# Kernel optimization log

Measured on AMD Instinct MI355X. Metric: run time of the kernel, lower is better.

## Reference

```python
import jax, jax.numpy as jnp
import numpy as np

N = 4096   # query tokens
M = 4096   # key/value tokens
D = 512    # embedding_dim


def setup_inputs() -> dict:
    key = jax.random.key(0)
    kq, kk, kv = jax.random.split(key, 3)
    return {
        "query": jax.random.normal(kq, (N, D), dtype=jnp.float32),
        "key": jax.random.normal(kk, (M, D), dtype=jnp.float32),
        "value": jax.random.normal(kv, (M, D), dtype=jnp.float32),
    }


def reference(query, key, value):
    # scores = Q K^T  (no 1/sqrt(d) scaling in the original module)
    attention_scores = jnp.einsum("nd,md->nm", query, key)  # [N, M]
    attention_probs = jax.nn.softmax(attention_scores, axis=-1)  # [N, M]
    output = jnp.einsum("nm,md->nd", attention_probs, value)  # [N, D]
    return (output, attention_probs)
```

## Files before the change

kernel.cpp:

```cpp
#include <hip/hip_runtime.h>
#include <hip/hip_bf16.h>
#include <stdint.h>

#define N_Q 4096
#define N_K 4096
#define DIM 512

typedef float f32x4 __attribute__((ext_vector_type(4)));
typedef __bf16 bf16x8 __attribute__((ext_vector_type(8)));
typedef unsigned short u16x4 __attribute__((ext_vector_type(4)));
typedef unsigned short u16x8 __attribute__((ext_vector_type(8)));

__device__ __forceinline__ f32x4 mfma_bf16(bf16x8 a, bf16x8 b, f32x4 c) {
  return __builtin_amdgcn_mfma_f32_16x16x32_bf16(a, b, c, 0, 0, 0);
}

__device__ __forceinline__ void gload16(const void* g, void* l) {
  __builtin_amdgcn_global_load_lds((const __attribute__((address_space(1))) void*)g,
                                   (__attribute__((address_space(3))) void*)l,
                                   16, 0, 0);
}

__device__ __forceinline__ void split4(const f32x4 v, u16x4& h, u16x4& l) {
#pragma unroll
  for (int i = 0; i < 4; ++i) {
    float f = v[i];
    uint32_t u = __builtin_bit_cast(uint32_t, f);
    uint32_t hb = (u + 0x8000u) & 0xffff0000u;
    float hf = __builtin_bit_cast(float, hb);
    float lf = f - hf;
    h[i] = (unsigned short)(hb >> 16);
    l[i] = (unsigned short)(__builtin_bit_cast(uint32_t, lf) >> 16);
  }
}

__device__ __forceinline__ unsigned short bf16r(float f) {
  uint32_t u = __builtin_bit_cast(uint32_t, f);
  return (unsigned short)((u + 0x8000u) >> 16);
}

__global__ __launch_bounds__(256) void split_kernel(const float* __restrict__ X,
                                                    unsigned short* __restrict__ X2) {
  const size_t base = ((size_t)blockIdx.x * 256 + threadIdx.x) * 8;
  const size_t row = base >> 9;
  const size_t col = base & 511;
  u16x8 H, L;
#pragma unroll
  for (int h = 0; h < 2; ++h) {
    f32x4 v = *(const f32x4*)(X + base + h * 4);
    u16x4 hh, ll;
    split4(v, hh, ll);
#pragma unroll
    for (int j = 0; j < 4; ++j) { H[h * 4 + j] = hh[j]; L[h * 4 + j] = ll[j]; }
  }
  *(u16x8*)(X2 + row * 1024 + col) = H;
  *(u16x8*)(X2 + row * 1024 + 512 + col) = L;
}

__global__ __launch_bounds__(256, 2) void qk2_kernel(const unsigned short* __restrict__ Xq,
                                                     const unsigned short* __restrict__ Xk,
                                                     float* __restrict__ S) {
  __shared__ __align__(16) char smem[65536];

  const int tid = threadIdx.x;
  const int lane = tid & 63, wid = tid >> 6;
  const int wr = wid >> 1, wc = wid & 1;

  const int bid = blockIdx.x;
  const int b = (bid & 7) * 128 + (bid >> 3);
  const int rbase = (b >> 5) * 128;
  const int cbase = (b & 31) * 128;

  const int lrow = lane >> 3;
  const int lchk = lane & 7;

  const f32x4 fzero = {0.f, 0.f, 0.f, 0.f};
  f32x4 acc[4][4];
#pragma unroll
  for (int m = 0; m < 4; ++m)
#pragma unroll
    for (int n = 0; n < 4; ++n) acc[m][n] = fzero;

  auto stage = [&](int buf, int t) {
#pragma unroll
    for (int i = 0; i < 4; ++i) {
      const int r = (wid << 5) + (i << 3) + lrow;
      const int sc = lchk ^ (r & 7);
      const unsigned short* g =
          Xq + (size_t)(rbase + r) * 1024 + (sc >> 2) * 512 + t * 32 + (sc & 3) * 8;
      uint32_t off = (uint32_t)(buf * 32768 + (((wid << 5) + (i << 3)) << 7));
      off = (uint32_t)__builtin_amdgcn_readfirstlane((int)off);
      gload16(g, smem + off);
    }
#pragma unroll
    for (int i = 0; i < 4; ++i) {
      const int r = (wid << 5) + (i << 3) + lrow;
      const int sc = lchk ^ (r & 7);
      const unsigned short* g =
          Xk + (size_t)(cbase + r) * 1024 + (sc >> 2) * 512 + t * 32 + (sc & 3) * 8;
      uint32_t off = (uint32_t)(buf * 32768 + 16384 + (((wid << 5) + (i << 3)) << 7));
      off = (uint32_t)__builtin_amdgcn_readfirstlane((int)off);
      gload16(g, smem + off);
    }
  };

  auto compute = [&](int buf) {
    const char* bA = smem + buf * 32768;
    const char* bB = bA + 16384;
    bf16x8 ah[4], al[4], bh[4], bl[4];
#pragma unroll
    for (int m = 0; m < 4; ++m) {
      int row = (wr << 6) + (m << 4) + (lane & 15);
      int ch = (lane >> 4) ^ (row & 7);
      int cl = (4 + (lane >> 4)) ^ (row & 7);
      ah[m] = *(const bf16x8*)(bA + row * 128 + ch * 16);
      al[m] = *(const bf16x8*)(bA + row * 128 + cl * 16);
    }
#pragma unroll
    for (int n = 0; n < 4; ++n) {
      int row = (wc << 6) + (n << 4) + (lane & 15);
      int ch = (lane >> 4) ^ (row & 7);
      int cl = (4 + (lane >> 4)) ^ (row & 7);
      bh[n] = *(const bf16x8*)(bB + row * 128 + ch * 16);
      bl[n] = *(const bf16x8*)(bB + row * 128 + cl * 16);
    }
#pragma unroll
    for (int m = 0; m < 4; ++m)
#pragma unroll
      for (int n = 0; n < 4; ++n) {
        acc[m][n] = mfma_bf16(ah[m], bh[n], acc[m][n]);
        acc[m][n] = mfma_bf16(ah[m], bl[n], acc[m][n]);
        acc[m][n] = mfma_bf16(al[m], bh[n], acc[m][n]);
      }
  };

  stage(0, 0);
  __syncthreads();
  int cur = 0;
  for (int t = 0; t < 16; ++t) {
    if (t + 1 < 16) stage(cur ^ 1, t + 1);
    compute(cur);
    __syncthreads();
    cur ^= 1;
  }

#pragma unroll
  for (int m = 0; m < 4; ++m) {
    int row = rbase + wr * 64 + m * 16 + (lane >> 4) * 4;
#pragma unroll
    for (int n = 0; n < 4; ++n) {
      int col = cbase + wc * 64 + n * 16 + (lane & 15);
#pragma unroll
      for (int j = 0; j < 4; ++j)
        S[(size_t)(row + j) * N_K + col] = acc[m][n][j];
    }
  }
}

__global__ __launch_bounds__(256, 2) void qk_kernel(const float* __restrict__ Q,
                                                    const float* __restrict__ K,
                                                    float* __restrict__ S) {
  __shared__ __align__(16) char sAh[16384];
  __shared__ __align__(16) char sAl[16384];
  __shared__ __align__(16) char sBh[16384];
  __shared__ __align__(16) char sBl[16384];

  const int tid = threadIdx.x;
  const int rbase = blockIdx.y * 128;
  const int cbase = blockIdx.x * 128;
  const int lane = tid & 63, wid = tid >> 6;
  const int wr = wid >> 1, wc = wid & 1;
  const int lr = lane & 15, lk = (lane >> 4) * 8;

  const int srow = tid >> 4;
  const int scol = (tid & 15) * 4;

  f32x4 qr[8], kr[8];
#pragma unroll
  for (int p = 0; p < 8; ++p) {
    int r = p * 16 + srow;
    qr[p] = *(const f32x4*)(Q + (size_t)(rbase + r) * DIM + scol);
    kr[p] = *(const f32x4*)(K + (size_t)(cbase + r) * DIM + scol);
  }

  const f32x4 fzero = {0.f, 0.f, 0.f, 0.f};
  f32x4 acc[4][4];
#pragma unroll
  for (int m = 0; m < 4; ++m)
#pragma unroll
    for (int n = 0; n < 4; ++n) acc[m][n] = fzero;

  for (int kk = 0; kk < DIM / 64; ++kk) {
    __syncthreads();
#pragma unroll
    for (int p = 0; p < 8; ++p) {
      int r = p * 16 + srow;
      uint32_t bo = (uint32_t)(r * 128) + (uint32_t)((scol * 2) ^ ((r & 7) << 4));
      u16x4 qh, ql, kh, kl;
      split4(qr[p], qh, ql);
      split4(kr[p], kh, kl);
      *(u16x4*)(sAh + bo) = qh;
      *(u16x4*)(sAl + bo) = ql;
      *(u16x4*)(sBh + bo) = kh;
      *(u16x4*)(sBl + bo) = kl;
    }
    __syncthreads();
    if (kk < DIM / 64 - 1) {
#pragma unroll
      for (int p = 0; p < 8; ++p) {
        int r = p * 16 + srow;
        qr[p] = *(const f32x4*)(Q + (size_t)(rbase + r) * DIM + (kk + 1) * 64 + scol);
        kr[p] = *(const f32x4*)(K + (size_t)(cbase + r) * DIM + (kk + 1) * 64 + scol);
      }
    }
#pragma unroll
    for (int kh = 0; kh < 2; ++kh) {
      bf16x8 a_h[4], a_l[4], b_h[4], b_l[4];
#pragma unroll
      for (int m = 0; m < 4; ++m) {
        int row = wr * 64 + m * 16 + lr;
        uint32_t co = (uint32_t)(((kh * 32 + lk) * 2) ^ ((row & 7) << 4));
        a_h[m] = *(const bf16x8*)(sAh + row * 128 + co);
        a_l[m] = *(const bf16x8*)(sAl + row * 128 + co);
      }
#pragma unroll
      for (int n = 0; n < 4; ++n) {
        int row = wc * 64 + n * 16 + lr;
        uint32_t co = (uint32_t)(((kh * 32 + lk) * 2) ^ ((row & 7) << 4));
        b_h[n] = *(const bf16x8*)(sBh + row * 128 + co);
        b_l[n] = *(const bf16x8*)(sBl + row * 128 + co);
      }
#pragma unroll
      for (int m = 0; m < 4; ++m)
#pragma unroll
        for (int n = 0; n < 4; ++n) {
          acc[m][n] = mfma_bf16(a_h[m], b_h[n], acc[m][n]);
          acc[m][n] = mfma_bf16(a_h[m], b_l[n], acc[m][n]);
          acc[m][n] = mfma_bf16(a_l[m], b_h[n], acc[m][n]);
        }
    }
  }

#pragma unroll
  for (int m = 0; m < 4; ++m) {
    int row = rbase + wr * 64 + m * 16 + (lane >> 4) * 4;
#pragma unroll
    for (int n = 0; n < 4; ++n) {
      int col = cbase + wc * 64 + n * 16 + lr;
#pragma unroll
      for (int j = 0; j < 4; ++j)
        S[(size_t)(row + j) * N_K + col] = acc[m][n][j];
    }
  }
}

__global__ __launch_bounds__(256) void softmax_kernel(float* __restrict__ P,
                                                      unsigned short* __restrict__ Pb) {
  const int tid = threadIdx.x;
  const int wid = tid >> 6, lane = tid & 63;
  float* p = P + (size_t)blockIdx.x * N_K;

  f32x4 v[4];
  float mx = -3.0e38f;
#pragma unroll
  for (int i = 0; i < 4; ++i) {
    v[i] = *(const f32x4*)(p + i * 1024 + tid * 4);
    mx = fmaxf(mx, fmaxf(fmaxf(v[i][0], v[i][1]), fmaxf(v[i][2], v[i][3])));
  }
#pragma unroll
  for (int o = 32; o > 0; o >>= 1) mx = fmaxf(mx, __shfl_xor(mx, o, 64));
  __shared__ float redM[4];
  __shared__ float redS[4];
  if (lane == 0) redM[wid] = mx;
  __syncthreads();
  mx = fmaxf(fmaxf(redM[0], redM[1]), fmaxf(redM[2], redM[3]));

  float s = 0.f;
#pragma unroll
  for (int i = 0; i < 4; ++i) {
#pragma unroll
    for (int j = 0; j < 4; ++j) {
      v[i][j] = __expf(v[i][j] - mx);
      s += v[i][j];
    }
  }
#pragma unroll
  for (int o = 32; o > 0; o >>= 1) s += __shfl_xor(s, o, 64);
  if (lane == 0) redS[wid] = s;
  __syncthreads();
  s = redS[0] + redS[1] + redS[2] + redS[3];
  const float inv = 1.0f / s;

  unsigned short* pb = Pb ? (Pb + (size_t)blockIdx.x * N_K) : nullptr;
#pragma unroll
  for (int i = 0; i < 4; ++i) {
    v[i] *= inv;
    *(f32x4*)(p + i * 1024 + tid * 4) = v[i];
    if (pb) {
      u16x4 h;
#pragma unroll
      for (int j = 0; j < 4; ++j) h[j] = bf16r(v[i][j]);
      *(u16x4*)(pb + i * 1024 + tid * 4) = h;
    }
  }
}

__global__ __launch_bounds__(256) void vt_kernel(const float* __restrict__ V,
                                                 unsigned short* __restrict__ Vt) {
  __shared__ unsigned short t[64][72];
  const int tid = threadIdx.x;
  const int d0 = blockIdx.x * 64;
  const int k0 = blockIdx.y * 64;

#pragma unroll
  for (int c = 0; c < 4; ++c) {
    int kr = (tid >> 4) + c * 16;
    f32x4 v = *(const f32x4*)(V + (size_t)(k0 + kr) * DIM + d0 + (tid & 15) * 4);
#pragma unroll
    for (int j = 0; j < 4; ++j) t[(tid & 15) * 4 + j][kr] = bf16r(v[j]);
  }
  __syncthreads();
#pragma unroll
  for (int c = 0; c < 2; ++c) {
    int d = (tid >> 3) + c * 32;
    int k = (tid & 7) * 8;
    *(uint4*)(Vt + (size_t)(d0 + d) * N_K + k0 + k) = *(const uint4*)&t[d][k];
  }
}

__global__ __launch_bounds__(256, 2) void pv3_kernel(const unsigned short* __restrict__ Pb,
                                                     const unsigned short* __restrict__ Vt,
                                                     float* __restrict__ Opart,
                                                     int kspan) {
  __shared__ __align__(16) char smem[65536];

  const int tid = threadIdx.x;
  const int lane = tid & 63, wid = tid >> 6;
  const int wr = wid >> 1, wc = wid & 1;
  const int rbase = blockIdx.y * 128;
  const int cbase = blockIdx.x * 128;
  const int k0 = blockIdx.z * kspan;
  float* Out = Opart + (size_t)blockIdx.z * ((size_t)N_Q * DIM);

  const int lrow = lane >> 3;
  const int lchk = lane & 7;
  const int iters = kspan >> 6;

  const f32x4 fzero = {0.f, 0.f, 0.f, 0.f};
  f32x4 acc[4][4];
#pragma unroll
  for (int m = 0; m < 4; ++m)
#pragma unroll
    for (int n = 0; n < 4; ++n) acc[m][n] = fzero;

  auto stage = [&](int buf, int t) {
    const size_t kel = (size_t)k0 + ((size_t)t << 6);
#pragma unroll
    for (int i = 0; i < 4; ++i) {
      const int rr = (wid << 5) + (i << 3) + lrow;
      const int gc = lchk ^ (rr & 7);
      const void* gA = (const void*)(Pb + (size_t)(rbase + rr) * N_K + kel + (gc << 3));
      uint32_t off = (uint32_t)(buf * 32768 + (((wid << 5) + (i << 3)) << 7));
      off = (uint32_t)__builtin_amdgcn_readfirstlane((int)off);
      gload16(gA, smem + off);
    }
#pragma unroll
    for (int i = 0; i < 4; ++i) {
      const int rr = (wid << 5) + (i << 3) + lrow;
      const int gc = lchk ^ (rr & 7);
      const void* gB = (const void*)(Vt + (size_t)(cbase + rr) * N_K + kel + (gc << 3));
      uint32_t off = (uint32_t)(buf * 32768 + 16384 + (((wid << 5) + (i << 3)) << 7));
      off = (uint32_t)__builtin_amdgcn_readfirstlane((int)off);
      gload16(gB, smem + off);
    }
  };

  auto compute = [&](int buf) {
    const char* bA = smem + buf * 32768;
    const char* bB = bA + 16384;
#pragma unroll
    for (int kh = 0; kh < 2; ++kh) {
      bf16x8 a[4], b[4];
#pragma unroll
      for (int m = 0; m < 4; ++m) {
        int row = (wr << 6) + (m << 4) + (lane & 15);
        uint32_t co = (uint32_t)(((((kh << 2) + (lane >> 4)) << 4)) ^ ((row & 7) << 4));
        a[m] = *(const bf16x8*)(bA + row * 128 + co);
      }
#pragma unroll
      for (int n = 0; n < 4; ++n) {
        int row = (wc << 6) + (n << 4) + (lane & 15);
        uint32_t co = (uint32_t)(((((kh << 2) + (lane >> 4)) << 4)) ^ ((row & 7) << 4));
        b[n] = *(const bf16x8*)(bB + row * 128 + co);
      }
#pragma unroll
      for (int m = 0; m < 4; ++m)
#pragma unroll
        for (int n = 0; n < 4; ++n)
          acc[m][n] = mfma_bf16(a[m], b[n], acc[m][n]);
    }
  };

  stage(0, 0);
  __syncthreads();
  int cur = 0;
  for (int t = 0; t < iters; ++t) {
    if (t + 1 < iters) stage(cur ^ 1, t + 1);
    compute(cur);
    __syncthreads();
    cur ^= 1;
  }

#pragma unroll
  for (int m = 0; m < 4; ++m) {
    int row = rbase + wr * 64 + m * 16 + (lane >> 4) * 4;
#pragma unroll
    for (int n = 0; n < 4; ++n) {
      int col = cbase + wc * 64 + n * 16 + (lane & 15);
#pragma unroll
      for (int j = 0; j < 4; ++j)
        Out[(size_t)(row + j) * DIM + col] = acc[m][n][j];
    }
  }
}

__global__ __launch_bounds__(256) void reduce_kernel(float* __restrict__ O,
                                                     const float* __restrict__ Opart,
                                                     int nsplit) {
  size_t i = ((size_t)blockIdx.x * 256 + threadIdx.x) * 4;
  f32x4 s = *(const f32x4*)(Opart + i);
  for (int z = 1; z < nsplit; ++z)
    s += *(const f32x4*)(Opart + (size_t)z * ((size_t)N_Q * DIM) + i);
  *(f32x4*)(O + i) = s;
}

__global__ __launch_bounds__(512, 2) void pv_kernel(const float* __restrict__ P,
                                                    const float* __restrict__ V,
                                                    float* __restrict__ O) {
  __shared__ __align__(16) char sA[16384];
  __shared__ __align__(16) char sB[16384];

  const int tid = threadIdx.x;
  const int rbase = blockIdx.y * 128;
  const int cbase = blockIdx.x * 128;
  const int lane = tid & 63, wid = tid >> 6;
  const int wr = wid >> 2, wc = wid & 3;
  const int lr = lane & 15, lk = (lane >> 4) * 8;

  const int a_row = tid >> 4;
  const int a_col = (tid & 15) * 4;
  const int b_c = tid & 127;
  const int b_oct = tid >> 7;

  f32x4 areg[4];
  float breg[4][4];
#pragma unroll
  for (int p = 0; p < 4; ++p) {
    int r = p * 32 + a_row;
    areg[p] = *(const f32x4*)(P + (size_t)(rbase + r) * N_K + a_col);
  }
#pragma unroll
  for (int g = 0; g < 4; ++g) {
    int kr0 = b_oct * 4 + g * 16;
#pragma unroll
    for (int i = 0; i < 4; ++i)
      breg[g][i] = V[(size_t)(kr0 + i) * DIM + cbase + b_c];
  }

  const f32x4 fzero = {0.f, 0.f, 0.f, 0.f};
  f32x4 acc[4][2];
#pragma unroll
  for (int m = 0; m < 4; ++m)
#pragma unroll
    for (int n = 0; n < 2; ++n) acc[m][n] = fzero;

  for (int kk = 0; kk < N_K / 64; ++kk) {
    __syncthreads();
#pragma unroll
    for (int p = 0; p < 4; ++p) {
      int r = p * 32 + a_row;
      uint32_t bo = (uint32_t)(r * 128) + (uint32_t)((a_col * 2) ^ ((r & 7) << 4));
      u16x4 hv;
#pragma unroll
      for (int i = 0; i < 4; ++i) hv[i] = bf16r(areg[p][i]);
      *(u16x4*)(sA + bo) = hv;
    }
#pragma unroll
    for (int g = 0; g < 4; ++g) {
      int kr0 = b_oct * 4 + g * 16;
      uint32_t bo = (uint32_t)(b_c * 128) + (uint32_t)((kr0 * 2) ^ ((b_c & 7) << 4));
      u16x4 hv;
#pragma unroll
      for (int i = 0; i < 4; ++i) hv[i] = bf16r(breg[g][i]);
      *(u16x4*)(sB + bo) = hv;
    }
    __syncthreads();
    if (kk < N_K / 64 - 1) {
#pragma unroll
      for (int p = 0; p < 4; ++p) {
        int r = p * 32 + a_row;
        areg[p] = *(const f32x4*)(P + (size_t)(rbase + r) * N_K + (kk + 1) * 64 + a_col);
      }
#pragma unroll
      for (int g = 0; g < 4; ++g) {
        int kr0 = b_oct * 4 + g * 16;
#pragma unroll
        for (int i = 0; i < 4; ++i)
          breg[g][i] = V[(size_t)((kk + 1) * 64 + kr0 + i) * DIM + cbase + b_c];
      }
    }
#pragma unroll
    for (int kh = 0; kh < 2; ++kh) {
      bf16x8 af[4], bf[2];
#pragma unroll
      for (int m = 0; m < 4; ++m) {
        int row = wr * 64 + m * 16 + lr;
        uint32_t co = (uint32_t)(((kh * 32 + lk) * 2) ^ ((row & 7) << 4));
        af[m] = *(const bf16x8*)(sA + row * 128 + co);
      }
#pragma unroll
      for (int n = 0; n < 2; ++n) {
        int row = wc * 32 + n * 16 + lr;
        uint32_t co = (uint32_t)(((kh * 32 + lk) * 2) ^ ((row & 7) << 4));
        bf[n] = *(const bf16x8*)(sB + row * 128 + co);
      }
#pragma unroll
      for (int m = 0; m < 4; ++m)
#pragma unroll
        for (int n = 0; n < 2; ++n)
          acc[m][n] = mfma_bf16(af[m], bf[n], acc[m][n]);
    }
  }

#pragma unroll
  for (int m = 0; m < 4; ++m) {
    int row = rbase + wr * 64 + m * 16 + (lane >> 4) * 4;
#pragma unroll
    for (int n = 0; n < 2; ++n) {
      int col = cbase + wc * 32 + n * 16 + lr;
#pragma unroll
      for (int j = 0; j < 4; ++j)
        O[(size_t)(row + j) * DIM + col] = acc[m][n][j];
    }
  }
}

extern "C" void kernel_launch(void* const* d_in, const int* in_sizes, int n_in,
                              void* d_out, int out_size, void* d_ws, size_t ws_size,
                              hipStream_t stream) {
  const float* Q = (const float*)d_in[0];
  const float* K = (const float*)d_in[1];
  const float* V = (const float*)d_in[2];
  float* O = (float*)d_out;
  float* P = O + (size_t)N_Q * DIM;

  const size_t PB_BYTES = (size_t)N_Q * N_K * 2;
  const size_t VT_BYTES = (size_t)DIM * N_K * 2;
  const size_t OP_BYTES = (size_t)N_Q * DIM * 4;

  int nsplit = 0;
  if (ws_size >= PB_BYTES + VT_BYTES + 4 * OP_BYTES) nsplit = 4;
  else if (ws_size >= PB_BYTES + VT_BYTES + 2 * OP_BYTES) nsplit = 2;
  else if (ws_size >= PB_BYTES + VT_BYTES) nsplit = 1;

  if (nsplit > 0) {
    unsigned short* Xq = (unsigned short*)d_ws;
    unsigned short* Xk = Xq + (size_t)N_Q * 1024;
    unsigned short* Pb = (unsigned short*)d_ws;
    unsigned short* Vt = (unsigned short*)((char*)d_ws + PB_BYTES);
    float* Opart = (float*)((char*)d_ws + PB_BYTES + VT_BYTES);

    split_kernel<<<1024, 256, 0, stream>>>(Q, Xq);
    split_kernel<<<1024, 256, 0, stream>>>(K, Xk);
    vt_kernel<<<dim3(DIM / 64, N_K / 64), 256, 0, stream>>>(V, Vt);
    qk2_kernel<<<1024, 256, 0, stream>>>(Xq, Xk, P);
    softmax_kernel<<<N_Q, 256, 0, stream>>>(P, Pb);
    if (nsplit == 1) {
      pv3_kernel<<<dim3(DIM / 128, N_Q / 128, 1), 256, 0, stream>>>(Pb, Vt, O, N_K);
    } else {
      pv3_kernel<<<dim3(DIM / 128, N_Q / 128, nsplit), 256, 0, stream>>>(Pb, Vt, Opart, N_K / nsplit);
      reduce_kernel<<<(N_Q * DIM) / (256 * 4), 256, 0, stream>>>(O, Opart, nsplit);
    }
  } else {
    qk_kernel<<<dim3(N_K / 128, N_Q / 128), 256, 0, stream>>>(Q, K, P);
    softmax_kernel<<<N_Q, 256, 0, stream>>>(P, nullptr);
    pv_kernel<<<dim3(DIM / 128, N_Q / 128), 512, 0, stream>>>(P, V, O);
  }
}
```

Measured before the change: 131.4 us.

## Replace bf16 hi/lo split QK^T with per-row int8 two-level quantized MFMA

Q and K are now quantized per row into an int8 high part plus an int8 residual at 1/128 scale, with a per-row float scale. A single fused quant kernel replaces the two bf16 split launches. The QK^T GEMM uses the i8 16x16x64 MFMA and recombines the hh and cross accumulators with the row and column scales in the epilogue. This halves operand bytes and the K-loop trip count and uses the higher-throughput int8 matrix path. The cost is reduced score precision (about 15 effective bits relative to each row's max), which softmax with unscaled scores may amplify.

Result: faster. 111.0 us, median of 2 (-15.5%).

```diff
diff --git a/kernel.cpp b/kernel.cpp
--- a/kernel.cpp
+++ b/kernel.cpp
@@ -9,10 +9,14 @@
 typedef float f32x4 __attribute__((ext_vector_type(4)));
 typedef __bf16 bf16x8 __attribute__((ext_vector_type(8)));
 typedef unsigned short u16x4 __attribute__((ext_vector_type(4)));
-typedef unsigned short u16x8 __attribute__((ext_vector_type(8)));
+typedef int i32x4 __attribute__((ext_vector_type(4)));
 
 __device__ __forceinline__ f32x4 mfma_bf16(bf16x8 a, bf16x8 b, f32x4 c) {
   return __builtin_amdgcn_mfma_f32_16x16x32_bf16(a, b, c, 0, 0, 0);
+}
+
+__device__ __forceinline__ i32x4 mfma_i8(i32x4 a, i32x4 b, i32x4 c) {
+  return __builtin_amdgcn_mfma_i32_16x16x64_i8(a, b, c, 0, 0, 0);
 }
 
 __device__ __forceinline__ void gload16(const void* g, void* l) {
@@ -39,26 +43,61 @@
   return (unsigned short)((u + 0x8000u) >> 16);
 }
 
-__global__ __launch_bounds__(256) void split_kernel(const float* __restrict__ X,
-                                                    unsigned short* __restrict__ X2) {
-  const size_t base = ((size_t)blockIdx.x * 256 + threadIdx.x) * 8;
-  const size_t row = base >> 9;
-  const size_t col = base & 511;
-  u16x8 H, L;
-#pragma unroll
-  for (int h = 0; h < 2; ++h) {
-    f32x4 v = *(const f32x4*)(X + base + h * 4);
-    u16x4 hh, ll;
-    split4(v, hh, ll);
-#pragma unroll
-    for (int j = 0; j < 4; ++j) { H[h * 4 + j] = hh[j]; L[h * 4 + j] = ll[j]; }
-  }
-  *(u16x8*)(X2 + row * 1024 + col) = H;
-  *(u16x8*)(X2 + row * 1024 + 512 + col) = L;
-}
-
-__global__ __launch_bounds__(256, 2) void qk2_kernel(const unsigned short* __restrict__ Xq,
-                                                     const unsigned short* __restrict__ Xk,
+__global__ __launch_bounds__(256) void quant_kernel(const float* __restrict__ Q,
+                                                    const float* __restrict__ K,
+                                                    signed char* __restrict__ Xq8,
+                                                    signed char* __restrict__ Xk8,
+                                                    float* __restrict__ sclA,
+                                                    float* __restrict__ sclB) {
+  const float* X = blockIdx.y ? K : Q;
+  signed char* X8 = blockIdx.y ? Xk8 : Xq8;
+  float* scl = blockIdx.y ? sclB : sclA;
+
+  const int lane = threadIdx.x & 63;
+  const int row = blockIdx.x * 4 + (threadIdx.x >> 6);
+
+  f32x4 v[2];
+  v[0] = *(const f32x4*)(X + (size_t)row * DIM + lane * 8);
+  v[1] = *(const f32x4*)(X + (size_t)row * DIM + lane * 8 + 4);
+
+  float mx = 0.f;
+#pragma unroll
+  for (int u = 0; u < 2; ++u)
+#pragma unroll
+    for (int j = 0; j < 4; ++j) mx = fmaxf(mx, fabsf(v[u][j]));
+#pragma unroll
+  for (int o = 32; o > 0; o >>= 1) mx = fmaxf(mx, __shfl_xor(mx, o, 64));
+
+  const float s = fmaxf(mx, 1e-20f) * (1.0f / 127.0f);
+  const float rinv = 1.0f / s;
+  const float linv = 128.0f * rinv;
+
+  uint32_t hw[2], lw[2];
+#pragma unroll
+  for (int u = 0; u < 2; ++u) {
+    uint32_t hword = 0, lword = 0;
+#pragma unroll
+    for (int j = 0; j < 4; ++j) {
+      float x = v[u][j];
+      int h = __float2int_rn(x * rinv);
+      float r = x - s * (float)h;
+      int l = __float2int_rn(r * linv);
+      hword |= ((uint32_t)(h & 0xff)) << (8 * j);
+      lword |= ((uint32_t)(l & 0xff)) << (8 * j);
+    }
+    hw[u] = hword; lw[u] = lword;
+  }
+  uint2 hv; hv.x = hw[0]; hv.y = hw[1];
+  uint2 lv; lv.x = lw[0]; lv.y = lw[1];
+  *(uint2*)(X8 + (size_t)row * 1024 + lane * 8) = hv;
+  *(uint2*)(X8 + (size_t)row * 1024 + 512 + lane * 8) = lv;
+  if (lane == 0) scl[row] = s;
+}
+
+__global__ __launch_bounds__(256, 2) void qk3_kernel(const signed char* __restrict__ Xq8,
+                                                     const signed char* __restrict__ Xk8,
+                                                     const float* __restrict__ sclA,
+                                                     const float* __restrict__ sclB,
                                                      float* __restrict__ S) {
   __shared__ __align__(16) char smem[65536];
 
@@ -74,20 +113,20 @@
   const int lrow = lane >> 3;
   const int lchk = lane & 7;
 
-  const f32x4 fzero = {0.f, 0.f, 0.f, 0.f};
-  f32x4 acc[4][4];
+  const i32x4 izero = {0, 0, 0, 0};
+  i32x4 acc_hh[4][4], acc_x[4][4];
 #pragma unroll
   for (int m = 0; m < 4; ++m)
 #pragma unroll
-    for (int n = 0; n < 4; ++n) acc[m][n] = fzero;
+    for (int n = 0; n < 4; ++n) { acc_hh[m][n] = izero; acc_x[m][n] = izero; }
 
   auto stage = [&](int buf, int t) {
 #pragma unroll
     for (int i = 0; i < 4; ++i) {
       const int r = (wid << 5) + (i << 3) + lrow;
       const int sc = lchk ^ (r & 7);
-      const unsigned short* g =
-          Xq + (size_t)(rbase + r) * 1024 + (sc >> 2) * 512 + t * 32 + (sc & 3) * 8;
+      const int colb = (sc < 4) ? (t * 64 + sc * 16) : (512 + t * 64 + (sc & 3) * 16);
+      const signed char* g = Xq8 + (size_t)(rbase + r) * 1024 + colb;
       uint32_t off = (uint32_t)(buf * 32768 + (((wid << 5) + (i << 3)) << 7));
       off = (uint32_t)__builtin_amdgcn_readfirstlane((int)off);
       gload16(g, smem + off);
@@ -96,8 +135,8 @@
     for (int i = 0; i < 4; ++i) {
       const int r = (wid << 5) + (i << 3) + lrow;
       const int sc = lchk ^ (r & 7);
-      const unsigned short* g =
-          Xk + (size_t)(cbase + r) * 1024 + (sc >> 2) * 512 + t * 32 + (sc & 3) * 8;
+      const int colb = (sc < 4) ? (t * 64 + sc * 16) : (512 + t * 64 + (sc & 3) * 16);
+      const signed char* g = Xk8 + (size_t)(cbase + r) * 1024 + colb;
       uint32_t off = (uint32_t)(buf * 32768 + 16384 + (((wid << 5) + (i << 3)) << 7));
       off = (uint32_t)__builtin_amdgcn_readfirstlane((int)off);
       gload16(g, smem + off);
@@ -107,38 +146,35 @@
   auto compute = [&](int buf) {
     const char* bA = smem + buf * 32768;
     const char* bB = bA + 16384;
-    bf16x8 ah[4], al[4], bh[4], bl[4];
+    const int kc = lane >> 4;
+    i32x4 ah[4], al[4], bh[4], bl[4];
 #pragma unroll
     for (int m = 0; m < 4; ++m) {
       int row = (wr << 6) + (m << 4) + (lane & 15);
-      int ch = (lane >> 4) ^ (row & 7);
-      int cl = (4 + (lane >> 4)) ^ (row & 7);
-      ah[m] = *(const bf16x8*)(bA + row * 128 + ch * 16);
-      al[m] = *(const bf16x8*)(bA + row * 128 + cl * 16);
+      ah[m] = *(const i32x4*)(bA + row * 128 + ((kc ^ (row & 7)) << 4));
+      al[m] = *(const i32x4*)(bA + row * 128 + (((4 + kc) ^ (row & 7)) << 4));
     }
 #pragma unroll
     for (int n = 0; n < 4; ++n) {
       int row = (wc << 6) + (n << 4) + (lane & 15);
-      int ch = (lane >> 4) ^ (row & 7);
-      int cl = (4 + (lane >> 4)) ^ (row & 7);
-      bh[n] = *(const bf16x8*)(bB + row * 128 + ch * 16);
-      bl[n] = *(const bf16x8*)(bB + row * 128 + cl * 16);
+      bh[n] = *(const i32x4*)(bB + row * 128 + ((kc ^ (row & 7)) << 4));
+      bl[n] = *(const i32x4*)(bB + row * 128 + (((4 + kc) ^ (row & 7)) << 4));
     }
 #pragma unroll
     for (int m = 0; m < 4; ++m)
 #pragma unroll
       for (int n = 0; n < 4; ++n) {
-        acc[m][n] = mfma_bf16(ah[m], bh[n], acc[m][n]);
-        acc[m][n] = mfma_bf16(ah[m], bl[n], acc[m][n]);
-        acc[m][n] = mfma_bf16(al[m], bh[n], acc[m][n]);
+        acc_hh[m][n] = mfma_i8(ah[m], bh[n], acc_hh[m][n]);
+        acc_x[m][n]  = mfma_i8(ah[m], bl[n], acc_x[m][n]);
+        acc_x[m][n]  = mfma_i8(al[m], bh[n], acc_x[m][n]);
       }
   };
 
   stage(0, 0);
   __syncthreads();
   int cur = 0;
-  for (int t = 0; t < 16; ++t) {
-    if (t + 1 < 16) stage(cur ^ 1, t + 1);
+  for (int t = 0; t < 8; ++t) {
+    if (t + 1 < 8) stage(cur ^ 1, t + 1);
     compute(cur);
     __syncthreads();
     cur ^= 1;
@@ -146,13 +182,19 @@
 
 #pragma unroll
   for (int m = 0; m < 4; ++m) {
-    int row = rbase + wr * 64 + m * 16 + (lane >> 4) * 4;
+    int row0 = rbase + wr * 64 + m * 16 + (lane >> 4) * 4;
+    float sa[4];
+#pragma unroll
+    for (int j = 0; j < 4; ++j) sa[j] = sclA[row0 + j];
 #pragma unroll
     for (int n = 0; n < 4; ++n) {
       int col = cbase + wc * 64 + n * 16 + (lane & 15);
-#pragma unroll
-      for (int j = 0; j < 4; ++j)
-        S[(size_t)(row + j) * N_K + col] = acc[m][n][j];
+      float sb = sclB[col];
+#pragma unroll
+      for (int j = 0; j < 4; ++j) {
+        float f = (float)acc_hh[m][n][j] + (float)acc_x[m][n][j] * 0.0078125f;
+        S[(size_t)(row0 + j) * N_K + col] = sa[j] * sb * f;
+      }
     }
   }
 }
@@ -556,24 +598,27 @@
 
   const size_t PB_BYTES = (size_t)N_Q * N_K * 2;
   const size_t VT_BYTES = (size_t)DIM * N_K * 2;
+  const size_t SCL_BYTES = 65536;
   const size_t OP_BYTES = (size_t)N_Q * DIM * 4;
 
   int nsplit = 0;
-  if (ws_size >= PB_BYTES + VT_BYTES + 4 * OP_BYTES) nsplit = 4;
-  else if (ws_size >= PB_BYTES + VT_BYTES + 2 * OP_BYTES) nsplit = 2;
-  else if (ws_size >= PB_BYTES + VT_BYTES) nsplit = 1;
+  if (ws_size >= PB_BYTES + VT_BYTES + SCL_BYTES + 4 * OP_BYTES) nsplit = 4;
+  else if (ws_size >= PB_BYTES + VT_BYTES + SCL_BYTES + 2 * OP_BYTES) nsplit = 2;
+  else if (ws_size >= PB_BYTES + VT_BYTES + SCL_BYTES) nsplit = 1;
 
   if (nsplit > 0) {
-    unsigned short* Xq = (unsigned short*)d_ws;
-    unsigned short* Xk = Xq + (size_t)N_Q * 1024;
-    unsigned short* Pb = (unsigned short*)d_ws;
-    unsigned short* Vt = (unsigned short*)((char*)d_ws + PB_BYTES);
-    float* Opart = (float*)((char*)d_ws + PB_BYTES + VT_BYTES);
-
-    split_kernel<<<1024, 256, 0, stream>>>(Q, Xq);
-    split_kernel<<<1024, 256, 0, stream>>>(K, Xk);
+    char* wsb = (char*)d_ws;
+    signed char* Xq8 = (signed char*)wsb;
+    signed char* Xk8 = Xq8 + (size_t)N_Q * 1024;
+    unsigned short* Pb = (unsigned short*)wsb;
+    unsigned short* Vt = (unsigned short*)(wsb + PB_BYTES);
+    float* sclA = (float*)(wsb + PB_BYTES + VT_BYTES);
+    float* sclB = sclA + N_Q;
+    float* Opart = (float*)(wsb + PB_BYTES + VT_BYTES + SCL_BYTES);
+
+    quant_kernel<<<dim3(N_Q / 4, 2), 256, 0, stream>>>(Q, K, Xq8, Xk8, sclA, sclB);
     vt_kernel<<<dim3(DIM / 64, N_K / 64), 256, 0, stream>>>(V, Vt);
-    qk2_kernel<<<1024, 256, 0, stream>>>(Xq, Xk, P);
+    qk3_kernel<<<1024, 256, 0, stream>>>(Xq8, Xk8, sclA, sclB, P);
     softmax_kernel<<<N_Q, 256, 0, stream>>>(P, Pb);
     if (nsplit == 1) {
       pv3_kernel<<<dim3(DIM / 128, N_Q / 128, 1), 256, 0, stream>>>(Pb, Vt, O, N_K);
```
